# Kernel optimization log

Hardware: AMD Instinct MI355X
Metric: run time of the kernel (lower is better)

Reference implementation:

```python
import jax, jax.numpy as jnp
import numpy as np

WEIGHT_LOC = 1.0
WEIGHT_FEAT = 1.0
TOP_K = 16  # feat_vector[:16].mean() in the original
EPS = 1e-12  # F.normalize default eps


def _l2_normalize(x, axis):
    return x / jnp.maximum(jnp.linalg.norm(x, axis=axis, keepdims=True), EPS)


def _pair_sim(gfa, cda, gfb, cdb):
    # gfa, gfb: (N, F) already row-normalized; cda, cdb: (N, 2)
    n = gfa.shape[0]
    # diagonal of gfa @ gfb.T (trace/gate in the original is computed but unused)
    v = jnp.sum(gfa * gfb, axis=-1)              # (N,)
    vs = -jnp.sort(-v)                            # sort descending
    sim_feat = jnp.mean(vs[:TOP_K])
    w = vs - jnp.min(vs)
    weight = (w[:, None] * w[None, :]).reshape(-1)          # (N*N,) outer product
    weight = weight / jnp.maximum(jnp.linalg.norm(weight), EPS)
    da = cda[:, None, :] - cda[None, :, :]        # (N, N, 2)
    db = cdb[:, None, :] - cdb[None, :, :]        # (N, N, 2)
    loc_dis = jnp.sum((da - db) ** 2, axis=-1).reshape(-1)  # (N*N,)
    dis_loc = jnp.mean(loc_dis * weight)
    return WEIGHT_FEAT * sim_feat - WEIGHT_LOC * dis_loc


def setup_inputs() -> dict:
    key = jax.random.key(0)
    k1, k2, k3, k4 = jax.random.split(key, 4)
    R, N, F = 8, 1024, 256
    return {
        "graph_feat_a": jax.random.normal(k1, (R, N, F), dtype=jnp.float32),
        "coord_a": jax.random.uniform(k2, (R, N, 2), dtype=jnp.float32),
        "graph_feat_b": jax.random.normal(k3, (R, N, F), dtype=jnp.float32),
        "coord_b": jax.random.uniform(k4, (R, N, 2), dtype=jnp.float32),
    }


def reference(graph_feat_a, coord_a, graph_feat_b, coord_b):
    gfa = _l2_normalize(graph_feat_a, axis=-1)  # F.normalize(gf, dim=1) on (N,F)
    gfb = _l2_normalize(graph_feat_b, axis=-1)
    # vectorize the original double Python loop over (N_rot_a, N_rot_b) pairs
    inner = jax.vmap(_pair_sim, in_axes=(None, None, 0, 0))
    outer = jax.vmap(inner, in_axes=(0, 0, None, None))
    sims = outer(gfa, coord_a, gfb, coord_b)    # (R, R)
    return jnp.max(sims)
```

## Files before the change

### kernel.cpp

```cpp
#include <hip/hip_runtime.h>
#include <math.h>

#define EPS 1e-12f

constexpr int N = 1024;
constexpr int F = 256;
constexpr int NPAIR = 64;

template <int CTRL>
__device__ __forceinline__ float dppAdd(float x) {
    int y = __builtin_amdgcn_update_dpp(0, __float_as_int(x), CTRL, 0xf, 0xf, true);
    return x + __int_as_float(y);
}
__device__ __forceinline__ float waveSum64(float x) {
    x = dppAdd<0x111>(x);
    x = dppAdd<0x112>(x);
    x = dppAdd<0x114>(x);
    x = dppAdd<0x118>(x);
    x = dppAdd<0x142>(x);
    x = dppAdd<0x143>(x);
    return x;
}

__device__ inline void atomicMaxFloat(float* addr, float val) {
    unsigned int* ua = (unsigned int*)addr;
    unsigned int old = __hip_atomic_load(ua, __ATOMIC_RELAXED, __HIP_MEMORY_SCOPE_AGENT);
    while (__uint_as_float(old) < val) {
        unsigned int assumed = old;
        old = atomicCAS(ua, assumed, __float_as_uint(val));
        if (old == assumed) break;
    }
}

__global__ __launch_bounds__(256) void dot_kernel(const float* __restrict__ gfa,
                                                  const float* __restrict__ gfb,
                                                  float* __restrict__ v,
                                                  float* __restrict__ out) {
    const int n = blockIdx.x;
    const int t = threadIdx.x;
    __shared__ float4 rows[16][64];
    __shared__ float invn[16];

    if (n == 0 && t == 0) out[0] = -INFINITY;

    #pragma unroll
    for (int rep = 0; rep < 4; ++rep) {
        const int idx = rep * 256 + t;
        const int row = idx >> 6;
        const int c4  = idx & 63;
        const float* src = (row < 8) ? gfa + ((size_t)row * N + n) * F
                                     : gfb + ((size_t)(row - 8) * N + n) * F;
        rows[row][c4] = ((const float4*)src)[c4];
    }
    __syncthreads();

    const int wave = t >> 6, lane = t & 63;

    #pragma unroll
    for (int rr = 0; rr < 4; ++rr) {
        const int row = wave * 4 + rr;
        const float4 a = rows[row][lane];
        float ss = a.x * a.x + a.y * a.y + a.z * a.z + a.w * a.w;
        #pragma unroll
        for (int off = 32; off; off >>= 1) ss += __shfl_down(ss, off);
        if (lane == 0) invn[row] = 1.f / fmaxf(sqrtf(ss), EPS);
    }
    __syncthreads();

    float4 b[8];
    #pragma unroll
    for (int rb = 0; rb < 8; ++rb) b[rb] = rows[8 + rb][lane];

    #pragma unroll
    for (int rr = 0; rr < 2; ++rr) {
        const int ra = wave * 2 + rr;
        const float4 a = rows[ra][lane];
        #pragma unroll
        for (int rb = 0; rb < 8; ++rb) {
            float d = a.x * b[rb].x + a.y * b[rb].y + a.z * b[rb].z + a.w * b[rb].w;
            #pragma unroll
            for (int off = 32; off; off >>= 1) d += __shfl_down(d, off);
            if (lane == 0)
                v[(size_t)(ra * 8 + rb) * N + n] = d * invn[ra] * invn[8 + rb];
        }
    }
}

__global__ __launch_bounds__(256) void pair_kernel(const float* __restrict__ v,
                                                   const float* __restrict__ ca,
                                                   const float* __restrict__ cb,
                                                   float* __restrict__ out) {
    const int p = blockIdx.x;
    const int ra = p >> 3, rb = p & 7;
    const int tid = threadIdx.x;
    const int lane = tid & 63, wv = tid >> 6;
    __shared__ float s[N];
    __shared__ float rbuf[4][6];

    const float4* pa4 = (const float4*)(ca + (size_t)ra * N * 2) + tid * 2;
    const float4* pb4 = (const float4*)(cb + (size_t)rb * N * 2) + tid * 2;
    const float4 a01 = pa4[0], a23 = pa4[1];
    const float4 b01 = pb4[0], b23 = pb4[1];

    const float4 xv = ((const float4*)(v + (size_t)p * N))[tid];
    float x[4] = { xv.x, xv.y, xv.z, xv.w };

    #pragma unroll
    for (int k = 2; k <= 1024; k <<= 1) {
        #pragma unroll
        for (int j = k >> 1; j >= 1; j >>= 1) {
            if (j >= 256) {
                ((float4*)s)[tid] = make_float4(x[0], x[1], x[2], x[3]);
                __syncthreads();
                const float4 yv = ((const float4*)s)[tid ^ (j >> 2)];
                const float y[4] = { yv.x, yv.y, yv.z, yv.w };
                const bool up = ((tid & (k >> 2)) == 0);
                const bool hi = ((tid & (j >> 2)) != 0);
                const bool keepMin = (hi != up);
                #pragma unroll
                for (int e = 0; e < 4; ++e)
                    x[e] = keepMin ? fminf(x[e], y[e]) : fmaxf(x[e], y[e]);
                __syncthreads();
            } else if (j >= 4) {
                const int J = j >> 2;
                const bool up = ((tid & (k >> 2)) == 0);
                const bool hi = ((lane & J) != 0);
                const bool keepMin = (hi != up);
                #pragma unroll
                for (int e = 0; e < 4; ++e) {
                    const float y = __shfl_xor(x[e], J);
                    x[e] = keepMin ? fminf(x[e], y) : fmaxf(x[e], y);
                }
            } else if (j == 2) {
                #pragma unroll
                for (int e = 0; e < 2; ++e) {
                    const int f = e + 2;
                    const bool up = (((tid * 4 + e) & k) == 0);
                    const float a = x[e], b2 = x[f];
                    x[e] = up ? fminf(a, b2) : fmaxf(a, b2);
                    x[f] = up ? fmaxf(a, b2) : fminf(a, b2);
                }
            } else {
                #pragma unroll
                for (int e = 0; e < 4; e += 2) {
                    const int f = e + 1;
                    const bool up = (((tid * 4 + e) & k) == 0);
                    const float a = x[e], b2 = x[f];
                    x[e] = up ? fminf(a, b2) : fmaxf(a, b2);
                    x[f] = up ? fmaxf(a, b2) : fminf(a, b2);
                }
            }
        }
    }

    ((float4*)s)[tid] = make_float4(x[0], x[1], x[2], x[3]);
    __syncthreads();

    const float vmin = s[0];
    const float4 dsc = ((const float4*)s)[255 - tid];
    const float u[4] = { dsc.w - vmin, dsc.z - vmin, dsc.y - vmin, dsc.x - vmin };

    float t16p = 0.f;
    if (tid < 4) {
        const float4 q = ((const float4*)s)[252 + tid];
        t16p = q.x + q.y + q.z + q.w;
    }

    float Su = 0.f, U2 = 0.f, A = 0.f, Bx = 0.f, By = 0.f;
    {
        const float ex0 = a01.x - b01.x, ey0 = a01.y - b01.y;
        const float ex1 = a01.z - b01.z, ey1 = a01.w - b01.w;
        const float ex2 = a23.x - b23.x, ey2 = a23.y - b23.y;
        const float ex3 = a23.z - b23.z, ey3 = a23.w - b23.w;
        const float exs[4] = { ex0, ex1, ex2, ex3 };
        const float eys[4] = { ey0, ey1, ey2, ey3 };
        #pragma unroll
        for (int e = 0; e < 4; ++e) {
            const float uu = u[e], ex = exs[e], ey = eys[e];
            Su += uu; U2 += uu * uu;
            A  += uu * (ex * ex + ey * ey);
            Bx += uu * ex; By += uu * ey;
        }
    }

    float vals[6] = { Su, U2, A, Bx, By, t16p };
    #pragma unroll
    for (int m = 0; m < 6; ++m) {
        const float r = waveSum64(vals[m]);
        if (lane == 63) rbuf[wv][m] = r;
    }
    __syncthreads();

    if (tid == 0) {
        float acc[6];
        #pragma unroll
        for (int m = 0; m < 6; ++m)
            acc[m] = rbuf[0][m] + rbuf[1][m] + rbuf[2][m] + rbuf[3][m];
        const float sim_feat = acc[5] * (1.f / 16.f);
        const float denom = (float)N * (float)N * fmaxf(acc[1], EPS);
        const float dis_loc = (2.f * acc[0] * acc[2] - 2.f * (acc[3] * acc[3] + acc[4] * acc[4])) / denom;
        atomicMaxFloat(out, sim_feat - dis_loc);
    }
}

extern "C" void kernel_launch(void* const* d_in, const int* in_sizes, int n_in,
                              void* d_out, int out_size, void* d_ws, size_t ws_size,
                              hipStream_t stream) {
    const float* gfa = (const float*)d_in[0];
    const float* ca  = (const float*)d_in[1];
    const float* gfb = (const float*)d_in[2];
    const float* cb  = (const float*)d_in[3];
    float* out = (float*)d_out;

    float* v = (float*)d_ws;

    dot_kernel<<<N, 256, 0, stream>>>(gfa, gfb, v, out);
    pair_kernel<<<NPAIR, 256, 0, stream>>>(v, ca, cb, out);
}
```

Before: 20.71 us.

## Pack four rows per dot block and replace shuffle reductions with DPP sums

The dot kernel now processes four node indices per 1024-thread block, launching 256 blocks instead of 1024. The separate norm pass, its shared-memory broadcast and the second barrier are gone: each wave computes its own norms and dot products with DPP-based wave reductions and writes results from lane 63. This cuts block scheduling overhead, barriers and shuffle-reduction latency. The cost is redundant norm computation across waves, more registers per thread and fewer, larger blocks across the CUs.

```diff
diff --git a/kernel.cpp b/kernel.cpp
--- a/kernel.cpp
+++ b/kernel.cpp
@@ -22,6 +22,10 @@
     return x;
 }
 
+__device__ __forceinline__ float dot4(float4 a, float4 b) {
+    return a.x * b.x + a.y * b.y + a.z * b.z + a.w * b.w;
+}
+
 __device__ inline void atomicMaxFloat(float* addr, float val) {
     unsigned int* ua = (unsigned int*)addr;
     unsigned int old = __hip_atomic_load(ua, __ATOMIC_RELAXED, __HIP_MEMORY_SCOPE_AGENT);
@@ -32,56 +36,57 @@
     }
 }
 
-__global__ __launch_bounds__(256) void dot_kernel(const float* __restrict__ gfa,
-                                                  const float* __restrict__ gfb,
-                                                  float* __restrict__ v,
-                                                  float* __restrict__ out) {
-    const int n = blockIdx.x;
-    const int t = threadIdx.x;
-    __shared__ float4 rows[16][64];
-    __shared__ float invn[16];
-
-    if (n == 0 && t == 0) out[0] = -INFINITY;
+__global__ __launch_bounds__(1024) void dot_kernel(const float* __restrict__ gfa,
+                                                   const float* __restrict__ gfb,
+                                                   float* __restrict__ v,
+                                                   float* __restrict__ out) {
+    __shared__ float4 rows[4][16][64];
+    const unsigned b    = blockIdx.x;
+    const unsigned tid  = threadIdx.x;
+    const unsigned sub  = tid >> 8;
+    const unsigned t    = tid & 255;
+    const unsigned lane = tid & 63;
+    const unsigned wv   = t >> 6;
+    const unsigned n    = b * 4 + sub;
+
+    if (b == 0 && tid == 0)
+        __hip_atomic_store(out, -INFINITY, __ATOMIC_RELAXED, __HIP_MEMORY_SCOPE_AGENT);
 
     #pragma unroll
     for (int rep = 0; rep < 4; ++rep) {
-        const int idx = rep * 256 + t;
+        const int idx = rep * 256 + (int)t;
         const int row = idx >> 6;
         const int c4  = idx & 63;
         const float* src = (row < 8) ? gfa + ((size_t)row * N + n) * F
                                      : gfb + ((size_t)(row - 8) * N + n) * F;
-        rows[row][c4] = ((const float4*)src)[c4];
+        rows[sub][row][c4] = ((const float4*)src)[c4];
     }
     __syncthreads();
 
-    const int wave = t >> 6, lane = t & 63;
-
-    #pragma unroll
-    for (int rr = 0; rr < 4; ++rr) {
-        const int row = wave * 4 + rr;
-        const float4 a = rows[row][lane];
-        float ss = a.x * a.x + a.y * a.y + a.z * a.z + a.w * a.w;
-        #pragma unroll
-        for (int off = 32; off; off >>= 1) ss += __shfl_down(ss, off);
-        if (lane == 0) invn[row] = 1.f / fmaxf(sqrtf(ss), EPS);
-    }
-    __syncthreads();
-
-    float4 b[8];
-    #pragma unroll
-    for (int rb = 0; rb < 8; ++rb) b[rb] = rows[8 + rb][lane];
-
-    #pragma unroll
-    for (int rr = 0; rr < 2; ++rr) {
-        const int ra = wave * 2 + rr;
-        const float4 a = rows[ra][lane];
+    const int ra0 = 2 * (int)wv, ra1 = ra0 + 1;
+    const float4 a0 = rows[sub][ra0][lane];
+    const float4 a1 = rows[sub][ra1][lane];
+    float4 bb[8];
+    #pragma unroll
+    for (int rb = 0; rb < 8; ++rb) bb[rb] = rows[sub][8 + rb][lane];
+
+    float na0 = waveSum64(dot4(a0, a0));
+    float na1 = waveSum64(dot4(a1, a1));
+    float nb[8], d0[8], d1[8];
+    #pragma unroll
+    for (int rb = 0; rb < 8; ++rb) {
+        nb[rb] = waveSum64(dot4(bb[rb], bb[rb]));
+        d0[rb] = waveSum64(dot4(a0, bb[rb]));
+        d1[rb] = waveSum64(dot4(a1, bb[rb]));
+    }
+    if (lane == 63) {
+        const float ia0 = 1.f / fmaxf(sqrtf(na0), EPS);
+        const float ia1 = 1.f / fmaxf(sqrtf(na1), EPS);
         #pragma unroll
         for (int rb = 0; rb < 8; ++rb) {
-            float d = a.x * b[rb].x + a.y * b[rb].y + a.z * b[rb].z + a.w * b[rb].w;
-            #pragma unroll
-            for (int off = 32; off; off >>= 1) d += __shfl_down(d, off);
-            if (lane == 0)
-                v[(size_t)(ra * 8 + rb) * N + n] = d * invn[ra] * invn[8 + rb];
+            const float ib = 1.f / fmaxf(sqrtf(nb[rb]), EPS);
+            v[(size_t)(ra0 * 8 + rb) * N + n] = d0[rb] * ia0 * ib;
+            v[(size_t)(ra1 * 8 + rb) * N + n] = d1[rb] * ia1 * ib;
         }
     }
 }
@@ -168,12 +173,8 @@
 
     float Su = 0.f, U2 = 0.f, A = 0.f, Bx = 0.f, By = 0.f;
     {
-        const float ex0 = a01.x - b01.x, ey0 = a01.y - b01.y;
-        const float ex1 = a01.z - b01.z, ey1 = a01.w - b01.w;
-        const float ex2 = a23.x - b23.x, ey2 = a23.y - b23.y;
-        const float ex3 = a23.z - b23.z, ey3 = a23.w - b23.w;
-        const float exs[4] = { ex0, ex1, ex2, ex3 };
-        const float eys[4] = { ey0, ey1, ey2, ey3 };
+        const float exs[4] = { a01.x - b01.x, a01.z - b01.z, a23.x - b23.x, a23.z - b23.z };
+        const float eys[4] = { a01.y - b01.y, a01.w - b01.w, a23.y - b23.y, a23.w - b23.w };
         #pragma unroll
         for (int e = 0; e < 4; ++e) {
             const float uu = u[e], ex = exs[e], ey = eys[e];
@@ -214,6 +215,6 @@
 
     float* v = (float*)d_ws;
 
-    dot_kernel<<<N, 256, 0, stream>>>(gfa, gfb, v, out);
+    dot_kernel<<<256, 1024, 0, stream>>>(gfa, gfb, v, out);
     pair_kernel<<<NPAIR, 256, 0, stream>>>(v, ca, cb, out);
 }
```

After: 19.99 us. 3.5% less time.
